# Optimization experiments

Measured on AMD Instinct MI355X. Metric: run time of the kernel, lower is better.

Reference implementation:

```python
import jax, jax.numpy as jnp
import numpy as np

N_NODES = 100000
N_EDGES = 3200000
IN_CH = 256


def setup_inputs() -> dict:
    key = jax.random.key(0)
    k1, k2, k3 = jax.random.split(key, 3)
    x = jax.random.normal(k1, (N_NODES, IN_CH), dtype=jnp.float32)
    edge_index = jax.random.randint(k2, (2, N_EDGES), 0, N_NODES, dtype=jnp.int64)
    # GCNConv linear: weight [in_channels, 1] (applied as x @ W), bias [1]
    W = jax.random.normal(k3, (IN_CH, 1), dtype=jnp.float32) * (1.0 / np.sqrt(IN_CH))
    b = jnp.zeros((1,), dtype=jnp.float32)
    return {"x": x, "edge_index": edge_index, "W": W, "b": b}


def reference(x, edge_index, W, b):
    # PyG GCNConv(in, 1): h = x @ W; add self-loops; symmetric norm; scatter-add to target; + bias
    N = x.shape[0]
    self_loops = jnp.broadcast_to(jnp.arange(N, dtype=edge_index.dtype)[None, :], (2, N))
    ei = jnp.concatenate([edge_index, self_loops], axis=1)  # [2, E+N]
    src, dst = ei[0], ei[1]

    # degree computed at target (col) with unit edge weights, incl. self-loops
    deg = jax.ops.segment_sum(jnp.ones(ei.shape[1], dtype=x.dtype), dst, num_segments=N)
    deg_inv_sqrt = jnp.where(deg > 0, jax.lax.rsqrt(deg), 0.0)
    norm = deg_inv_sqrt[src] * deg_inv_sqrt[dst]  # [E+N]

    h = x @ W  # [N, 1] — project first (out_channels < in_channels)
    msg = norm[:, None] * h[src]  # [E+N, 1]
    out = jax.ops.segment_sum(msg, dst, num_segments=N)  # [N, 1]
    return out + b
```

## Files before the change

kernel.cpp:

```cpp
#include <hip/hip_runtime.h>

#define GCN_N 100000
#define GCN_E 3200000
#define GCN_C 256

#define BSHIFT 8
#define NBUCK 391
#define BCAP 10240
#define NB1 512
#define TB1 1024
#define CHUNK (GCN_E / NB1)
#define PERTHR ((CHUNK + TB1 - 1) / TB1)


__global__ void k_init_cursor(int* __restrict__ cursor) {
    const int p = blockIdx.x * blockDim.x + threadIdx.x;
    if (p < NBUCK) cursor[p] = p * BCAP;
}

__global__ void k_proj(const float* __restrict__ x, const float* __restrict__ W,
                       float* __restrict__ h, int n) {
    const int lane   = threadIdx.x & 63;
    const int wave   = (blockIdx.x * blockDim.x + threadIdx.x) >> 6;
    const int nwaves = (gridDim.x * blockDim.x) >> 6;
    const float4 wf = *reinterpret_cast<const float4*>(W + lane * 4);
    for (int i = wave; i < n; i += nwaves) {
        const float4 xv = *reinterpret_cast<const float4*>(x + (size_t)i * GCN_C + lane * 4);
        float s = xv.x * wf.x + xv.y * wf.y + xv.z * wf.z + xv.w * wf.w;
        #pragma unroll
        for (int off = 32; off > 0; off >>= 1)
            s += __shfl_down(s, off, 64);
        if (lane == 0) h[i] = s;
    }
}

__global__ void __launch_bounds__(TB1) k_bin(const int* __restrict__ src,
                                             const int* __restrict__ dst,
                                             int* __restrict__ cursor,
                                             int* __restrict__ bpack) {
    __shared__ int hist[NBUCK];
    __shared__ int base[NBUCK];
    __shared__ int lscan[512];
    __shared__ int spack[CHUNK];
    __shared__ int sdest[CHUNK];
    const int tid = threadIdx.x;

    for (int p = tid; p < NBUCK; p += TB1) hist[p] = 0;
    __syncthreads();

    const int c0 = blockIdx.x * CHUNK;
    int my_pack[PERTHR], my_bkt[PERTHR], my_off[PERTHR];
    #pragma unroll
    for (int j = 0; j < PERTHR; ++j) {
        const int k = tid + j * TB1;
        my_bkt[j] = -1;
        if (k < CHUNK) {
            const int d = dst[c0 + k];
            const int s = src[c0 + k];
            const int b = d >> BSHIFT;
            my_pack[j] = (s << BSHIFT) | (d & 255);
            my_bkt[j]  = b;
            my_off[j]  = atomicAdd(&hist[b], 1);
        }
    }
    __syncthreads();

    if (tid < NBUCK) base[tid] = atomicAdd(&cursor[tid], hist[tid]);
    if (tid < 512)   lscan[tid] = (tid < NBUCK) ? hist[tid] : 0;
    __syncthreads();
    for (int d = 1; d < 512; d <<= 1) {
        int v = 0;
        if (tid < 512 && tid >= d) v = lscan[tid - d];
        __syncthreads();
        if (tid < 512 && tid >= d) lscan[tid] += v;
        __syncthreads();
    }

    #pragma unroll
    for (int j = 0; j < PERTHR; ++j) {
        if (my_bkt[j] >= 0) {
            const int b    = my_bkt[j];
            const int slot = lscan[b] - hist[b] + my_off[j];
            const int gpos = base[b] + my_off[j];
            spack[slot] = my_pack[j];
            sdest[slot] = (gpos < (b + 1) * BCAP) ? gpos : -1;
        }
    }
    __syncthreads();

    for (int i = tid; i < CHUNK; i += TB1) {
        const int dpos = sdest[i];
        if (dpos >= 0) bpack[dpos] = spack[i];
    }
}

__global__ void __launch_bounds__(512) k_deg_norm(const int* __restrict__ bpack,
                                                  const int* __restrict__ cursor,
                                                  const float* __restrict__ h,
                                                  float* __restrict__ dis,
                                                  float* __restrict__ g) {
    __shared__ int cnt[256];
    const int p = blockIdx.x, tid = threadIdx.x;
    if (tid < 256) cnt[tid] = 0;
    __syncthreads();
    const int s0 = p * BCAP;
    const int s1 = min(cursor[p], (p + 1) * BCAP);
    for (int i = s0 + tid; i < s1; i += 512)
        atomicAdd(&cnt[bpack[i] & 255], 1);
    __syncthreads();
    if (tid < 256) {
        const int node = (p << BSHIFT) + tid;
        if (node < GCN_N) {
            const float r = rsqrtf(1.0f + (float)cnt[tid]);
            dis[node] = r;
            g[node]   = r * h[node];
        }
    }
}

__global__ void __launch_bounds__(512) k_scatter_bin(const int* __restrict__ bpack,
                                                     const int* __restrict__ cursor,
                                                     const float* __restrict__ g,
                                                     const float* __restrict__ dis,
                                                     const float* __restrict__ bias,
                                                     float* __restrict__ out) {
    __shared__ float acc[256];
    const int p = blockIdx.x, tid = threadIdx.x;
    if (tid < 256) acc[tid] = 0.0f;
    __syncthreads();
    const int s0 = p * BCAP;
    const int s1 = min(cursor[p], (p + 1) * BCAP);
    for (int i = s0 + tid; i < s1; i += 512) {
        const int pk = bpack[i];
        atomicAdd(&acc[pk & 255], g[pk >> BSHIFT]);
    }
    __syncthreads();
    if (tid < 256) {
        const int node = (p << BSHIFT) + tid;
        if (node < GCN_N)
            out[node] = bias[0] + dis[node] * (acc[tid] + g[node]);
    }
}


__global__ void k_zero(float* __restrict__ a, int n) {
    int i = blockIdx.x * blockDim.x + threadIdx.x;
    const int stride = gridDim.x * blockDim.x;
    for (; i < n; i += stride) a[i] = 0.0f;
}
__global__ void k_degree_flat(const int* __restrict__ dst, float* __restrict__ deg, int e) {
    int i = blockIdx.x * blockDim.x + threadIdx.x;
    const int stride = gridDim.x * blockDim.x;
    for (; i < e; i += stride) atomicAdd(&deg[dst[i]], 1.0f);
}
__global__ void k_norm_flat(const float* __restrict__ h, float* __restrict__ deg_dis,
                            float* __restrict__ out, const float* __restrict__ bias, int n) {
    const int i = blockIdx.x * blockDim.x + threadIdx.x;
    if (i < n) {
        const float r = rsqrtf(deg_dis[i] + 1.0f);
        deg_dis[i] = r;
        out[i] = bias[0] + r * r * h[i];
    }
}
__global__ void k_scatter_flat(const int* __restrict__ src, const int* __restrict__ dst,
                               const float* __restrict__ h, const float* __restrict__ dis,
                               float* __restrict__ out, int e) {
    int i = blockIdx.x * blockDim.x + threadIdx.x;
    const int stride = gridDim.x * blockDim.x;
    for (; i < e; i += stride) {
        const int s = src[i], d = dst[i];
        atomicAdd(&out[d], dis[s] * dis[d] * h[s]);
    }
}

extern "C" void kernel_launch(void* const* d_in, const int* in_sizes, int n_in,
                              void* d_out, int out_size, void* d_ws, size_t ws_size,
                              hipStream_t stream) {
    const float* x  = (const float*)d_in[0];
    const int*   ei = (const int*)d_in[1];
    const float* W  = (const float*)d_in[2];
    const float* b  = (const float*)d_in[3];
    float* out = (float*)d_out;

    const int* src = ei;
    const int* dst = ei + GCN_E;

    const size_t need_bin = ((size_t)3 * GCN_N + NBUCK + (size_t)NBUCK * BCAP) * sizeof(float);
    if (ws_size >= need_bin) {
        float* h      = (float*)d_ws;
        float* dis    = h + GCN_N;
        float* g      = dis + GCN_N;
        int*   cursor = (int*)(g + GCN_N);
        int*   bpack  = cursor + NBUCK;

        k_init_cursor<<<(NBUCK + 255) / 256, 256, 0, stream>>>(cursor);
        k_proj<<<2048, 256, 0, stream>>>(x, W, h, GCN_N);
        k_bin<<<NB1, TB1, 0, stream>>>(src, dst, cursor, bpack);
        k_deg_norm<<<NBUCK, 512, 0, stream>>>(bpack, cursor, h, dis, g);
        k_scatter_bin<<<NBUCK, 512, 0, stream>>>(bpack, cursor, g, dis, b, out);
    } else {
        float* h   = (float*)d_ws;
        float* deg = h + GCN_N;
        k_zero<<<512, 256, 0, stream>>>(deg, GCN_N);
        k_proj<<<2048, 256, 0, stream>>>(x, W, h, GCN_N);
        k_degree_flat<<<2048, 256, 0, stream>>>(dst, deg, GCN_E);
        k_norm_flat<<<(GCN_N + 255) / 256, 256, 0, stream>>>(h, deg, out, b, GCN_N);
        k_scatter_flat<<<2048, 256, 0, stream>>>(src, dst, h, deg, out, GCN_E);
    }
}
```

Baseline: 78.19 us.

## Fuse projection into binning kernel via block specialization; wave-shuffle scan; wider blocks

```diff
diff --git a/kernel.cpp b/kernel.cpp
--- a/kernel.cpp
+++ b/kernel.cpp
@@ -7,6 +7,7 @@
 #define BSHIFT 8
 #define NBUCK 391
 #define BCAP 10240
+#define NBP 128
 #define NB1 512
 #define TB1 1024
 #define CHUNK (GCN_E / NB1)
@@ -18,37 +19,41 @@
     if (p < NBUCK) cursor[p] = p * BCAP;
 }
 
-__global__ void k_proj(const float* __restrict__ x, const float* __restrict__ W,
-                       float* __restrict__ h, int n) {
-    const int lane   = threadIdx.x & 63;
-    const int wave   = (blockIdx.x * blockDim.x + threadIdx.x) >> 6;
-    const int nwaves = (gridDim.x * blockDim.x) >> 6;
-    const float4 wf = *reinterpret_cast<const float4*>(W + lane * 4);
-    for (int i = wave; i < n; i += nwaves) {
-        const float4 xv = *reinterpret_cast<const float4*>(x + (size_t)i * GCN_C + lane * 4);
-        float s = xv.x * wf.x + xv.y * wf.y + xv.z * wf.z + xv.w * wf.w;
-        #pragma unroll
-        for (int off = 32; off > 0; off >>= 1)
-            s += __shfl_down(s, off, 64);
-        if (lane == 0) h[i] = s;
-    }
-}
-
-__global__ void __launch_bounds__(TB1) k_bin(const int* __restrict__ src,
-                                             const int* __restrict__ dst,
-                                             int* __restrict__ cursor,
-                                             int* __restrict__ bpack) {
+__global__ void __launch_bounds__(TB1) k_proj_bin(const float* __restrict__ x,
+                                                  const float* __restrict__ W,
+                                                  float* __restrict__ h,
+                                                  const int* __restrict__ src,
+                                                  const int* __restrict__ dst,
+                                                  int* __restrict__ cursor,
+                                                  int* __restrict__ bpack) {
     __shared__ int hist[NBUCK];
     __shared__ int base[NBUCK];
-    __shared__ int lscan[512];
+    __shared__ int lscan[NBUCK];
+    __shared__ int wsum[16], woff[16];
     __shared__ int spack[CHUNK];
     __shared__ int sdest[CHUNK];
     const int tid = threadIdx.x;
 
+    if (blockIdx.x < NBP) {
+        const int lane = tid & 63;
+        const int wave = (blockIdx.x * TB1 + tid) >> 6;
+        const int nwaves = NBP * (TB1 / 64);
+        const float4 wf = *reinterpret_cast<const float4*>(W + lane * 4);
+        for (int i = wave; i < GCN_N; i += nwaves) {
+            const float4 xv = *reinterpret_cast<const float4*>(x + (size_t)i * GCN_C + lane * 4);
+            float s = xv.x * wf.x + xv.y * wf.y + xv.z * wf.z + xv.w * wf.w;
+            #pragma unroll
+            for (int off = 32; off > 0; off >>= 1)
+                s += __shfl_down(s, off, 64);
+            if (lane == 0) h[i] = s;
+        }
+        return;
+    }
+
     for (int p = tid; p < NBUCK; p += TB1) hist[p] = 0;
     __syncthreads();
 
-    const int c0 = blockIdx.x * CHUNK;
+    const int c0 = (blockIdx.x - NBP) * CHUNK;
     int my_pack[PERTHR], my_bkt[PERTHR], my_off[PERTHR];
     #pragma unroll
     for (int j = 0; j < PERTHR; ++j) {
@@ -66,15 +71,25 @@
     __syncthreads();
 
     if (tid < NBUCK) base[tid] = atomicAdd(&cursor[tid], hist[tid]);
-    if (tid < 512)   lscan[tid] = (tid < NBUCK) ? hist[tid] : 0;
-    __syncthreads();
-    for (int d = 1; d < 512; d <<= 1) {
-        int v = 0;
-        if (tid < 512 && tid >= d) v = lscan[tid - d];
+    {
+        const int lane = tid & 63, w = tid >> 6;
+        int v = (tid < NBUCK) ? hist[tid] : 0;
+        #pragma unroll
+        for (int d2 = 1; d2 < 64; d2 <<= 1) {
+            const int t = __shfl_up(v, d2, 64);
+            if (lane >= d2) v += t;
+        }
+        if (lane == 63) wsum[w] = v;
         __syncthreads();
-        if (tid < 512 && tid >= d) lscan[tid] += v;
+        if (tid < 16) {
+            int s = 0;
+            for (int k = 0; k < tid; ++k) s += wsum[k];
+            woff[tid] = s;
+        }
         __syncthreads();
-    }
+        if (tid < NBUCK) lscan[tid] = v + woff[w];
+    }
+    __syncthreads();
 
     #pragma unroll
     for (int j = 0; j < PERTHR; ++j) {
@@ -94,18 +109,18 @@
     }
 }
 
-__global__ void __launch_bounds__(512) k_deg_norm(const int* __restrict__ bpack,
-                                                  const int* __restrict__ cursor,
-                                                  const float* __restrict__ h,
-                                                  float* __restrict__ dis,
-                                                  float* __restrict__ g) {
+__global__ void __launch_bounds__(1024) k_deg_norm(const int* __restrict__ bpack,
+                                                   const int* __restrict__ cursor,
+                                                   const float* __restrict__ h,
+                                                   float* __restrict__ dis,
+                                                   float* __restrict__ g) {
     __shared__ int cnt[256];
     const int p = blockIdx.x, tid = threadIdx.x;
     if (tid < 256) cnt[tid] = 0;
     __syncthreads();
     const int s0 = p * BCAP;
     const int s1 = min(cursor[p], (p + 1) * BCAP);
-    for (int i = s0 + tid; i < s1; i += 512)
+    for (int i = s0 + tid; i < s1; i += 1024)
         atomicAdd(&cnt[bpack[i] & 255], 1);
     __syncthreads();
     if (tid < 256) {
@@ -118,19 +133,19 @@
     }
 }
 
-__global__ void __launch_bounds__(512) k_scatter_bin(const int* __restrict__ bpack,
-                                                     const int* __restrict__ cursor,
-                                                     const float* __restrict__ g,
-                                                     const float* __restrict__ dis,
-                                                     const float* __restrict__ bias,
-                                                     float* __restrict__ out) {
+__global__ void __launch_bounds__(1024) k_scatter_bin(const int* __restrict__ bpack,
+                                                      const int* __restrict__ cursor,
+                                                      const float* __restrict__ g,
+                                                      const float* __restrict__ dis,
+                                                      const float* __restrict__ bias,
+                                                      float* __restrict__ out) {
     __shared__ float acc[256];
     const int p = blockIdx.x, tid = threadIdx.x;
     if (tid < 256) acc[tid] = 0.0f;
     __syncthreads();
     const int s0 = p * BCAP;
     const int s1 = min(cursor[p], (p + 1) * BCAP);
-    for (int i = s0 + tid; i < s1; i += 512) {
+    for (int i = s0 + tid; i < s1; i += 1024) {
         const int pk = bpack[i];
         atomicAdd(&acc[pk & 255], g[pk >> BSHIFT]);
     }
@@ -147,6 +162,21 @@
     int i = blockIdx.x * blockDim.x + threadIdx.x;
     const int stride = gridDim.x * blockDim.x;
     for (; i < n; i += stride) a[i] = 0.0f;
+}
+__global__ void k_proj_sep(const float* __restrict__ x, const float* __restrict__ W,
+                           float* __restrict__ h, int n) {
+    const int lane   = threadIdx.x & 63;
+    const int wave   = (blockIdx.x * blockDim.x + threadIdx.x) >> 6;
+    const int nwaves = (gridDim.x * blockDim.x) >> 6;
+    const float4 wf = *reinterpret_cast<const float4*>(W + lane * 4);
+    for (int i = wave; i < n; i += nwaves) {
+        const float4 xv = *reinterpret_cast<const float4*>(x + (size_t)i * GCN_C + lane * 4);
+        float s = xv.x * wf.x + xv.y * wf.y + xv.z * wf.z + xv.w * wf.w;
+        #pragma unroll
+        for (int off = 32; off > 0; off >>= 1)
+            s += __shfl_down(s, off, 64);
+        if (lane == 0) h[i] = s;
+    }
 }
 __global__ void k_degree_flat(const int* __restrict__ dst, float* __restrict__ deg, int e) {
     int i = blockIdx.x * blockDim.x + threadIdx.x;
@@ -194,15 +224,14 @@
         int*   bpack  = cursor + NBUCK;
 
         k_init_cursor<<<(NBUCK + 255) / 256, 256, 0, stream>>>(cursor);
-        k_proj<<<2048, 256, 0, stream>>>(x, W, h, GCN_N);
-        k_bin<<<NB1, TB1, 0, stream>>>(src, dst, cursor, bpack);
-        k_deg_norm<<<NBUCK, 512, 0, stream>>>(bpack, cursor, h, dis, g);
-        k_scatter_bin<<<NBUCK, 512, 0, stream>>>(bpack, cursor, g, dis, b, out);
+        k_proj_bin<<<NBP + NB1, TB1, 0, stream>>>(x, W, h, src, dst, cursor, bpack);
+        k_deg_norm<<<NBUCK, 1024, 0, stream>>>(bpack, cursor, h, dis, g);
+        k_scatter_bin<<<NBUCK, 1024, 0, stream>>>(bpack, cursor, g, dis, b, out);
     } else {
         float* h   = (float*)d_ws;
         float* deg = h + GCN_N;
         k_zero<<<512, 256, 0, stream>>>(deg, GCN_N);
-        k_proj<<<2048, 256, 0, stream>>>(x, W, h, GCN_N);
+        k_proj_sep<<<2048, 256, 0, stream>>>(x, W, h, GCN_N);
         k_degree_flat<<<2048, 256, 0, stream>>>(dst, deg, GCN_E);
         k_norm_flat<<<(GCN_N + 255) / 256, 256, 0, stream>>>(h, deg, out, b, GCN_N);
         k_scatter_flat<<<2048, 256, 0, stream>>>(src, dst, h, deg, out, GCN_E);
```

Result: faster. 74.12 us (-5.2%).
